# Performance work log

Hardware: AMD Instinct MI355X
Metric: run time of the kernel (lower is better)

Reference implementation:

```python
import jax, jax.numpy as jnp
import numpy as np

MARGIN = 1.0  # cur_margin for LBA_inverted_loss=True
COS_SCALE = 128.0


def smoothed_metric_loss(X, margin=MARGIN):
    # X: [B, E]. Lifted structured loss with inverted cosine similarity.
    B = X.shape[0]
    P = B // 2
    D = (X @ X.T) / COS_SCALE            # [B, B]
    E = jnp.exp(margin + D)              # [B, B]
    # For pair p (rows i=2p, j=2p+1): sum E over rows {i,j}, all columns except {i,j}.
    Eb = E.reshape(P, 2, P, 2)           # [P, 2, P, 2]
    row_sums = Eb.sum(axis=(1, 2, 3))    # [P] full sum over both rows of pair p
    idx = jnp.arange(P)
    diag_block = Eb[idx, :, idx, :].sum(axis=(1, 2))  # [P] the excluded 2x2 block
    S = row_sums - diag_block            # [P] masked sums
    Dij = D.reshape(P, 2, P, 2)[idx, 0, idx, 1]       # [P] D[i, j]
    J = jnp.log(S) - Dij
    return 0.5 * jnp.mean(J * J)


def reference(text_embeddings, shape_embeddings):
    B = text_embeddings.shape[0]
    # shape_embeddings repeated twice per model: row k -> shape[k // 2]
    shape_rep = jnp.repeat(shape_embeddings, 2, axis=0)      # [B, E]
    metric_tt = smoothed_metric_loss(text_embeddings)
    # mask rows: even rows keep text, odd rows take repeated shape embedding
    even = (jnp.arange(B) % 2 == 0)[:, None]
    mixed = jnp.where(even, text_embeddings, shape_rep)      # [B, E]
    metric_st = smoothed_metric_loss(mixed)
    return metric_tt + metric_st


def setup_inputs() -> dict:
    key = jax.random.key(0)
    k1, k2 = jax.random.split(key)
    B, E = 8192, 128
    text_embeddings = jax.random.normal(k1, (B, E), dtype=jnp.float32)
    shape_embeddings = jax.random.normal(k2, (B // 2, E), dtype=jnp.float32)
    return {"text_embeddings": text_embeddings, "shape_embeddings": shape_embeddings}
```

## Files before the change

kernel.cpp:

```cpp
#include <hip/hip_runtime.h>
#include <hip/hip_bf16.h>


#define B_ROWS 8192
#define E_COLS 128
#define P_PAIRS 4096
#define NSTRIP 128
#define NH 8

using f32x4 = __attribute__((ext_vector_type(4))) float;
using i32x8 = __attribute__((ext_vector_type(8))) int;

#define BF_SCALE 0.106164482742544f
#define EULER    2.718281828459045f
#define SCALE1   0x7f

__device__ __forceinline__ unsigned pk4_fp8(float a, float b, float c, float d) {
    unsigned v = 0;
    v = __builtin_amdgcn_cvt_pk_fp8_f32(a * BF_SCALE, b * BF_SCALE, v, false);
    v = __builtin_amdgcn_cvt_pk_fp8_f32(c * BF_SCALE, d * BF_SCALE, v, true);
    return v;
}

__global__ void convert_kernel(const float* __restrict__ text,
                               const float* __restrict__ shape,
                               unsigned* __restrict__ Xt,
                               unsigned* __restrict__ Xm,
                               float* __restrict__ R,
                               float* __restrict__ out) {
    int idx = blockIdx.x * blockDim.x + threadIdx.x;
    if (idx < 4096) {
        float4 z; z.x = z.y = z.z = z.w = 0.f;
        ((float4*)R)[idx] = z;
    }
    if (idx == 0) *out = 0.f;
    int e = idx * 4;
    if (e >= B_ROWS * E_COLS) return;
    float4 t = *(const float4*)(text + e);
    unsigned tp = pk4_fp8(t.x, t.y, t.z, t.w);
    Xt[idx] = tp;
    int row = e >> 7;
    if (row & 1) {
        int col = e & 127;
        float4 s = *(const float4*)(shape + (row >> 1) * E_COLS + col);
        Xm[idx] = pk4_fp8(s.x, s.y, s.z, s.w);
    } else {
        Xm[idx] = tp;
    }
}

__device__ __forceinline__ int lds_off(int row, int k0) {
    return (row << 7) + (k0 ^ ((row & 7) << 4));
}

__device__ __forceinline__ i32x8 load_frag32(const char* base, int row, int k32) {
    union { i32x8 v; int4 h[2]; } u;
    u.h[0] = *(const int4*)(base + lds_off(row, k32));
    u.h[1] = *(const int4*)(base + lds_off(row, k32 + 16));
    return u.v;
}

__device__ __forceinline__ i32x8 load_frag32_g(const char* rowbase, int k32) {
    union { i32x8 v; int4 h[2]; } u;
    u.h[0] = *(const int4*)(rowbase + k32);
    u.h[1] = *(const int4*)(rowbase + k32 + 16);
    return u.v;
}

__device__ __forceinline__ void stage8k(const char* gsrc, char* ldst, int tid) {
#pragma unroll
    for (int it = 0; it < 2; ++it) {
        int L   = it * 4096 + tid * 16;
        int row = L >> 7;
        int cb  = L & 127;
        int src = (row << 7) + (cb ^ ((row & 7) << 4));
        __builtin_amdgcn_global_load_lds(
            (const __attribute__((address_space(1))) void*)(gsrc + src),
            (__attribute__((address_space(3))) void*)(ldst + L), 16, 0, 0);
    }
}

__launch_bounds__(256, 6)
__global__ void gemm_rowsum_kernel(const unsigned char* __restrict__ Xt,
                                   const unsigned char* __restrict__ Xm,
                                   float* __restrict__ R) {
    const int bm = blockIdx.x, h = blockIdx.y, l = blockIdx.z;
    const char* gX = (const char*)(l ? Xm : Xt);

    __shared__ __align__(16) char bufs[3][64 * 128];
    const int tid = threadIdx.x;

    const int t0 = (h == 0) ? NH : h;
    const int N  = (h == 0) ? (bm < 64 ? 8 : 7) : 8;

    stage8k(gX + (size_t)((bm + t0) & 127) * 8192, bufs[0], tid);
    stage8k(gX + (size_t)((bm + t0 + NH) & 127) * 8192, bufs[1], tid);

    const int lane = tid & 63;
    const int w  = tid >> 6;
    const int wr = w >> 1, wc = w & 1;
    const int rA0 = wr * 32 + (lane & 15);
    const int rB0 = wc * 32 + (lane & 15);
    const int k32 = (lane >> 4) * 32;

    const char* Ag = gX + (size_t)bm * 8192;
    i32x8 afr[2];
    afr[0] = load_frag32_g(Ag + (size_t)rA0 * 128, k32);
    afr[1] = load_frag32_g(Ag + (size_t)(rA0 + 16) * 128, k32);

    float s_r[2][4] = {{0.f}};

    if (h == 0) {
        i32x8 b0 = load_frag32_g(Ag + (size_t)rB0 * 128, k32);
        i32x8 b1 = load_frag32_g(Ag + (size_t)(rB0 + 16) * 128, k32);
        f32x4 acc[2][2] = {};
        acc[0][0] = __builtin_amdgcn_mfma_scale_f32_16x16x128_f8f6f4(
            afr[0], b0, acc[0][0], 0, 0, 0, SCALE1, 0, SCALE1);
        acc[0][1] = __builtin_amdgcn_mfma_scale_f32_16x16x128_f8f6f4(
            afr[0], b1, acc[0][1], 0, 0, 0, SCALE1, 0, SCALE1);
        acc[1][0] = __builtin_amdgcn_mfma_scale_f32_16x16x128_f8f6f4(
            afr[1], b0, acc[1][0], 0, 0, 0, SCALE1, 0, SCALE1);
        acc[1][1] = __builtin_amdgcn_mfma_scale_f32_16x16x128_f8f6f4(
            afr[1], b1, acc[1][1], 0, 0, 0, SCALE1, 0, SCALE1);
#pragma unroll
        for (int m = 0; m < 2; ++m)
#pragma unroll
            for (int n = 0; n < 2; ++n)
#pragma unroll
                for (int j = 0; j < 4; ++j)
                    s_r[m][j] += __builtin_amdgcn_exp2f(acc[m][n][j]);
    }

    asm volatile("s_waitcnt vmcnt(0)" ::: "memory");
    __builtin_amdgcn_s_barrier();

    for (int idx = 0; idx < N; ++idx) {
        if (idx + 2 < N)
            stage8k(gX + (size_t)((bm + t0 + NH * (idx + 2)) & 127) * 8192,
                    bufs[(idx + 2) % 3], tid);

        const char* lsrc = bufs[idx % 3];
        i32x8 bfr[2];
        bfr[0] = load_frag32(lsrc, rB0, k32);
        bfr[1] = load_frag32(lsrc, rB0 + 16, k32);

        f32x4 acc[2][2] = {};
        __builtin_amdgcn_s_setprio(1);
        acc[0][0] = __builtin_amdgcn_mfma_scale_f32_16x16x128_f8f6f4(
            afr[0], bfr[0], acc[0][0], 0, 0, 0, SCALE1, 0, SCALE1);
        acc[0][1] = __builtin_amdgcn_mfma_scale_f32_16x16x128_f8f6f4(
            afr[0], bfr[1], acc[0][1], 0, 0, 0, SCALE1, 0, SCALE1);
        acc[1][0] = __builtin_amdgcn_mfma_scale_f32_16x16x128_f8f6f4(
            afr[1], bfr[0], acc[1][0], 0, 0, 0, SCALE1, 0, SCALE1);
        acc[1][1] = __builtin_amdgcn_mfma_scale_f32_16x16x128_f8f6f4(
            afr[1], bfr[1], acc[1][1], 0, 0, 0, SCALE1, 0, SCALE1);
        __builtin_amdgcn_s_setprio(0);

        const int bn = (bm + t0 + NH * idx) & 127;
        float s_c[2] = {0.f, 0.f};
#pragma unroll
        for (int m = 0; m < 2; ++m)
#pragma unroll
            for (int n = 0; n < 2; ++n)
#pragma unroll
                for (int j = 0; j < 4; ++j) {
                    float e2 = __builtin_amdgcn_exp2f(acc[m][n][j]);
                    s_r[m][j] += e2;
                    s_c[n] += e2;
                }
#pragma unroll
        for (int n = 0; n < 2; ++n) {
            float v = s_c[n];
            v += __shfl_xor(v, 16, 64);
            v += __shfl_xor(v, 32, 64);
            if (lane < 16) {
                int gcol = bn * 64 + wc * 32 + n * 16 + lane;
                atomicAdd(&R[l * B_ROWS + gcol], EULER * v);
            }
        }

        if (idx + 1 < N) {
            asm volatile("s_waitcnt lgkmcnt(0)" ::: "memory");
            asm volatile("s_waitcnt vmcnt(4)" ::: "memory");
            __builtin_amdgcn_s_barrier();
        }
    }

#pragma unroll
    for (int m = 0; m < 2; ++m)
#pragma unroll
        for (int j = 0; j < 4; ++j) {
            float v = s_r[m][j];
            v += __shfl_xor(v, 1, 64);
            v += __shfl_xor(v, 2, 64);
            v += __shfl_xor(v, 4, 64);
            v += __shfl_xor(v, 8, 64);
            if ((lane & 15) == 0) {
                int grow = bm * 64 + wr * 32 + m * 16 + (lane >> 4) * 4 + j;
                atomicAdd(&R[l * B_ROWS + grow], EULER * v);
            }
        }
}

__global__ void finalize_kernel(const float* __restrict__ text,
                                const float* __restrict__ shape,
                                const float* __restrict__ R,
                                float* __restrict__ out) {
    const int tid = threadIdx.x;
    const int lane = tid & 63;
    const int w = tid >> 6;
    const int waveGlobal = blockIdx.x * 4 + w;
    const float inv128 = 0.0078125f;
    float accum = 0.f;

    for (int task = waveGlobal; task < 2 * P_PAIRS; task += 2048) {
        int l = task >> 12;
        int p = task & (P_PAIRS - 1);
        const float* a = text + (2 * p) * E_COLS;
        const float* b = l ? (shape + p * E_COLS) : (text + (2 * p + 1) * E_COLS);
        float2 av = *(const float2*)(a + lane * 2);
        float2 bv = *(const float2*)(b + lane * 2);
        float dii = av.x * av.x + av.y * av.y;
        float djj = bv.x * bv.x + bv.y * bv.y;
        float dij = av.x * bv.x + av.y * bv.y;
#pragma unroll
        for (int sh = 1; sh < 64; sh <<= 1) {
            dii += __shfl_xor(dii, sh, 64);
            djj += __shfl_xor(djj, sh, 64);
            dij += __shfl_xor(dij, sh, 64);
        }
        if (lane == 0) {
            float Dii = dii * inv128, Djj = djj * inv128, Dij = dij * inv128;
            float S = R[l * B_ROWS + 2 * p] + R[l * B_ROWS + 2 * p + 1]
                    - (__expf(1.f + Dii) + 2.f * __expf(1.f + Dij) + __expf(1.f + Djj));
            float J = __logf(S) - Dij;
            accum += 0.5f * J * J * (1.0f / (float)P_PAIRS);
        }
    }

    __shared__ float red[4];
    if (lane == 0) red[w] = accum;
    __syncthreads();
    if (tid == 0) {
        atomicAdd(out, red[0] + red[1] + red[2] + red[3]);
    }
}

extern "C" void kernel_launch(void* const* d_in, const int* in_sizes, int n_in,
                              void* d_out, int out_size, void* d_ws, size_t ws_size,
                              hipStream_t stream) {
    const float* text  = (const float*)d_in[0];
    const float* shape = (const float*)d_in[1];
    float* out = (float*)d_out;
    char* ws = (char*)d_ws;

    unsigned char* Xt = (unsigned char*)ws;
    unsigned char* Xm = (unsigned char*)(ws + 1u * 1024u * 1024u);
    float* R = (float*)(ws + 2u * 1024u * 1024u);

    convert_kernel<<<(B_ROWS * E_COLS / 4 + 255) / 256, 256, 0, stream>>>(
        text, shape, (unsigned*)Xt, (unsigned*)Xm, R, out);

    dim3 grid(NSTRIP, NH, 2);
    gemm_rowsum_kernel<<<grid, 256, 0, stream>>>(Xt, Xm, R);

    finalize_kernel<<<512, 256, 0, stream>>>(text, shape, R, out);
}
```

Before: 44.54 us.

## Double-tile LDS stages, fully unroll GEMM loop, defer column-sum atomics

The rowsum GEMM now stages two 64-row tiles per buffer slot across a triple buffer, and runs a fully unrolled four-phase loop with one barrier per pair of tiles. The variable trip count is replaced by a multiplier that zeroes the eighth tile for the blocks that skip it. Column-sum atomics are deferred until after all MFMA work. The aim is fewer barriers and waitcnt stalls and more loads in flight, at the cost of twice the LDS, a lower launch-bound occupancy hint and more live registers. The finalize kernel is also launched with half as many blocks, and the convert kernel's bounds check now runs before it zeroes R.

```diff
diff --git a/kernel.cpp b/kernel.cpp
--- a/kernel.cpp
+++ b/kernel.cpp
@@ -20,6 +20,37 @@
     v = __builtin_amdgcn_cvt_pk_fp8_f32(a * BF_SCALE, b * BF_SCALE, v, false);
     v = __builtin_amdgcn_cvt_pk_fp8_f32(c * BF_SCALE, d * BF_SCALE, v, true);
     return v;
+}
+
+__device__ __forceinline__ int lds_off(int row, int k0) {
+    return (row << 7) + (k0 ^ ((row & 7) << 4));
+}
+
+__device__ __forceinline__ i32x8 load_frag32(const char* base, int row, int k32) {
+    union { i32x8 v; int4 h[2]; } u;
+    u.h[0] = *(const int4*)(base + lds_off(row, k32));
+    u.h[1] = *(const int4*)(base + lds_off(row, k32 + 16));
+    return u.v;
+}
+
+__device__ __forceinline__ i32x8 load_frag32_g(const char* rowbase, int k32) {
+    union { i32x8 v; int4 h[2]; } u;
+    u.h[0] = *(const int4*)(rowbase + k32);
+    u.h[1] = *(const int4*)(rowbase + k32 + 16);
+    return u.v;
+}
+
+__device__ __forceinline__ void stage8k(const char* gsrc, char* ldst, int tid) {
+#pragma unroll
+    for (int it = 0; it < 2; ++it) {
+        int L   = it * 4096 + tid * 16;
+        int row = L >> 7;
+        int cb  = L & 127;
+        int src = (row << 7) + (cb ^ ((row & 7) << 4));
+        __builtin_amdgcn_global_load_lds(
+            (const __attribute__((address_space(1))) void*)(gsrc + src),
+            (__attribute__((address_space(3))) void*)(ldst + L), 16, 0, 0);
+    }
 }
 
 __global__ void convert_kernel(const float* __restrict__ text,
@@ -29,13 +60,13 @@
                                float* __restrict__ R,
                                float* __restrict__ out) {
     int idx = blockIdx.x * blockDim.x + threadIdx.x;
+    if (idx >= B_ROWS * E_COLS / 4) return;
     if (idx < 4096) {
         float4 z; z.x = z.y = z.z = z.w = 0.f;
         ((float4*)R)[idx] = z;
     }
     if (idx == 0) *out = 0.f;
     int e = idx * 4;
-    if (e >= B_ROWS * E_COLS) return;
     float4 t = *(const float4*)(text + e);
     unsigned tp = pk4_fp8(t.x, t.y, t.z, t.w);
     Xt[idx] = tp;
@@ -49,52 +80,18 @@
     }
 }
 
-__device__ __forceinline__ int lds_off(int row, int k0) {
-    return (row << 7) + (k0 ^ ((row & 7) << 4));
-}
-
-__device__ __forceinline__ i32x8 load_frag32(const char* base, int row, int k32) {
-    union { i32x8 v; int4 h[2]; } u;
-    u.h[0] = *(const int4*)(base + lds_off(row, k32));
-    u.h[1] = *(const int4*)(base + lds_off(row, k32 + 16));
-    return u.v;
-}
-
-__device__ __forceinline__ i32x8 load_frag32_g(const char* rowbase, int k32) {
-    union { i32x8 v; int4 h[2]; } u;
-    u.h[0] = *(const int4*)(rowbase + k32);
-    u.h[1] = *(const int4*)(rowbase + k32 + 16);
-    return u.v;
-}
-
-__device__ __forceinline__ void stage8k(const char* gsrc, char* ldst, int tid) {
-#pragma unroll
-    for (int it = 0; it < 2; ++it) {
-        int L   = it * 4096 + tid * 16;
-        int row = L >> 7;
-        int cb  = L & 127;
-        int src = (row << 7) + (cb ^ ((row & 7) << 4));
-        __builtin_amdgcn_global_load_lds(
-            (const __attribute__((address_space(1))) void*)(gsrc + src),
-            (__attribute__((address_space(3))) void*)(ldst + L), 16, 0, 0);
-    }
-}
-
-__launch_bounds__(256, 6)
+__launch_bounds__(256, 3)
 __global__ void gemm_rowsum_kernel(const unsigned char* __restrict__ Xt,
                                    const unsigned char* __restrict__ Xm,
                                    float* __restrict__ R) {
     const int bm = blockIdx.x, h = blockIdx.y, l = blockIdx.z;
     const char* gX = (const char*)(l ? Xm : Xt);
 
-    __shared__ __align__(16) char bufs[3][64 * 128];
+    __shared__ __align__(16) char bufs[3][2][64 * 128];
     const int tid = threadIdx.x;
 
     const int t0 = (h == 0) ? NH : h;
-    const int N  = (h == 0) ? (bm < 64 ? 8 : 7) : 8;
-
-    stage8k(gX + (size_t)((bm + t0) & 127) * 8192, bufs[0], tid);
-    stage8k(gX + (size_t)((bm + t0 + NH) & 127) * 8192, bufs[1], tid);
+    const float g7 = (h == 0 && bm >= 64) ? 0.f : 1.f;
 
     const int lane = tid & 63;
     const int w  = tid >> 6;
@@ -108,20 +105,32 @@
     afr[0] = load_frag32_g(Ag + (size_t)rA0 * 128, k32);
     afr[1] = load_frag32_g(Ag + (size_t)(rA0 + 16) * 128, k32);
 
+    i32x8 db0 = {}, db1 = {};
+    if (h == 0) {
+        db0 = load_frag32_g(Ag + (size_t)rB0 * 128, k32);
+        db1 = load_frag32_g(Ag + (size_t)(rB0 + 16) * 128, k32);
+    }
+
+    stage8k(gX + (size_t)((bm + t0)     & 127) * 8192, bufs[0][0], tid);
+    stage8k(gX + (size_t)((bm + t0 + 8) & 127) * 8192, bufs[0][1], tid);
+    stage8k(gX + (size_t)((bm + t0 + 16) & 127) * 8192, bufs[1][0], tid);
+    stage8k(gX + (size_t)((bm + t0 + 24) & 127) * 8192, bufs[1][1], tid);
+
+    asm volatile("s_waitcnt vmcnt(8)" ::: "memory");
+
     float s_r[2][4] = {{0.f}};
+    float sc[8][2];
 
     if (h == 0) {
-        i32x8 b0 = load_frag32_g(Ag + (size_t)rB0 * 128, k32);
-        i32x8 b1 = load_frag32_g(Ag + (size_t)(rB0 + 16) * 128, k32);
         f32x4 acc[2][2] = {};
         acc[0][0] = __builtin_amdgcn_mfma_scale_f32_16x16x128_f8f6f4(
-            afr[0], b0, acc[0][0], 0, 0, 0, SCALE1, 0, SCALE1);
+            afr[0], db0, acc[0][0], 0, 0, 0, SCALE1, 0, SCALE1);
         acc[0][1] = __builtin_amdgcn_mfma_scale_f32_16x16x128_f8f6f4(
-            afr[0], b1, acc[0][1], 0, 0, 0, SCALE1, 0, SCALE1);
+            afr[0], db1, acc[0][1], 0, 0, 0, SCALE1, 0, SCALE1);
         acc[1][0] = __builtin_amdgcn_mfma_scale_f32_16x16x128_f8f6f4(
-            afr[1], b0, acc[1][0], 0, 0, 0, SCALE1, 0, SCALE1);
+            afr[1], db0, acc[1][0], 0, 0, 0, SCALE1, 0, SCALE1);
         acc[1][1] = __builtin_amdgcn_mfma_scale_f32_16x16x128_f8f6f4(
-            afr[1], b1, acc[1][1], 0, 0, 0, SCALE1, 0, SCALE1);
+            afr[1], db1, acc[1][1], 0, 0, 0, SCALE1, 0, SCALE1);
 #pragma unroll
         for (int m = 0; m < 2; ++m)
 #pragma unroll
@@ -131,58 +140,67 @@
                     s_r[m][j] += __builtin_amdgcn_exp2f(acc[m][n][j]);
     }
 
-    asm volatile("s_waitcnt vmcnt(0)" ::: "memory");
-    __builtin_amdgcn_s_barrier();
-
-    for (int idx = 0; idx < N; ++idx) {
-        if (idx + 2 < N)
-            stage8k(gX + (size_t)((bm + t0 + NH * (idx + 2)) & 127) * 8192,
-                    bufs[(idx + 2) % 3], tid);
-
-        const char* lsrc = bufs[idx % 3];
-        i32x8 bfr[2];
-        bfr[0] = load_frag32(lsrc, rB0, k32);
-        bfr[1] = load_frag32(lsrc, rB0 + 16, k32);
-
-        f32x4 acc[2][2] = {};
-        __builtin_amdgcn_s_setprio(1);
-        acc[0][0] = __builtin_amdgcn_mfma_scale_f32_16x16x128_f8f6f4(
-            afr[0], bfr[0], acc[0][0], 0, 0, 0, SCALE1, 0, SCALE1);
-        acc[0][1] = __builtin_amdgcn_mfma_scale_f32_16x16x128_f8f6f4(
-            afr[0], bfr[1], acc[0][1], 0, 0, 0, SCALE1, 0, SCALE1);
-        acc[1][0] = __builtin_amdgcn_mfma_scale_f32_16x16x128_f8f6f4(
-            afr[1], bfr[0], acc[1][0], 0, 0, 0, SCALE1, 0, SCALE1);
-        acc[1][1] = __builtin_amdgcn_mfma_scale_f32_16x16x128_f8f6f4(
-            afr[1], bfr[1], acc[1][1], 0, 0, 0, SCALE1, 0, SCALE1);
-        __builtin_amdgcn_s_setprio(0);
-
-        const int bn = (bm + t0 + NH * idx) & 127;
-        float s_c[2] = {0.f, 0.f};
-#pragma unroll
-        for (int m = 0; m < 2; ++m)
-#pragma unroll
-            for (int n = 0; n < 2; ++n)
+#pragma unroll
+    for (int p = 0; p < 4; ++p) {
+        if (p < 3) { asm volatile("s_waitcnt vmcnt(4)" ::: "memory"); }
+        else       { asm volatile("s_waitcnt vmcnt(0)" ::: "memory"); }
+        __builtin_amdgcn_s_barrier();
+        if (p + 2 < 4) {
+            stage8k(gX + (size_t)((bm + t0 + 8 * (2 * p + 4)) & 127) * 8192,
+                    bufs[(p + 2) % 3][0], tid);
+            stage8k(gX + (size_t)((bm + t0 + 8 * (2 * p + 5)) & 127) * 8192,
+                    bufs[(p + 2) % 3][1], tid);
+        }
+
+#pragma unroll
+        for (int sub = 0; sub < 2; ++sub) {
+            const int k = 2 * p + sub;
+            const char* lsrc = bufs[p % 3][sub];
+            i32x8 bfr0 = load_frag32(lsrc, rB0, k32);
+            i32x8 bfr1 = load_frag32(lsrc, rB0 + 16, k32);
+
+            f32x4 acc[2][2] = {};
+            __builtin_amdgcn_s_setprio(1);
+            acc[0][0] = __builtin_amdgcn_mfma_scale_f32_16x16x128_f8f6f4(
+                afr[0], bfr0, acc[0][0], 0, 0, 0, SCALE1, 0, SCALE1);
+            acc[0][1] = __builtin_amdgcn_mfma_scale_f32_16x16x128_f8f6f4(
+                afr[0], bfr1, acc[0][1], 0, 0, 0, SCALE1, 0, SCALE1);
+            acc[1][0] = __builtin_amdgcn_mfma_scale_f32_16x16x128_f8f6f4(
+                afr[1], bfr0, acc[1][0], 0, 0, 0, SCALE1, 0, SCALE1);
+            acc[1][1] = __builtin_amdgcn_mfma_scale_f32_16x16x128_f8f6f4(
+                afr[1], bfr1, acc[1][1], 0, 0, 0, SCALE1, 0, SCALE1);
+            __builtin_amdgcn_s_setprio(0);
+
+            const float g = (k == 7) ? g7 : 1.f;
+            float c0 = 0.f, c1 = 0.f;
+#pragma unroll
+            for (int m = 0; m < 2; ++m)
 #pragma unroll
                 for (int j = 0; j < 4; ++j) {
-                    float e2 = __builtin_amdgcn_exp2f(acc[m][n][j]);
-                    s_r[m][j] += e2;
-                    s_c[n] += e2;
+                    float e0 = __builtin_amdgcn_exp2f(acc[m][0][j]) * g;
+                    float e1 = __builtin_amdgcn_exp2f(acc[m][1][j]) * g;
+                    s_r[m][j] += e0 + e1;
+                    c0 += e0;
+                    c1 += e1;
                 }
+            sc[k][0] = c0;
+            sc[k][1] = c1;
+        }
+        asm volatile("s_waitcnt lgkmcnt(0)" ::: "memory");
+    }
+
+#pragma unroll
+    for (int k = 0; k < 8; ++k) {
+        const int bn = (bm + t0 + 8 * k) & 127;
 #pragma unroll
         for (int n = 0; n < 2; ++n) {
-            float v = s_c[n];
+            float v = sc[k][n];
             v += __shfl_xor(v, 16, 64);
             v += __shfl_xor(v, 32, 64);
             if (lane < 16) {
                 int gcol = bn * 64 + wc * 32 + n * 16 + lane;
                 atomicAdd(&R[l * B_ROWS + gcol], EULER * v);
             }
-        }
-
-        if (idx + 1 < N) {
-            asm volatile("s_waitcnt lgkmcnt(0)" ::: "memory");
-            asm volatile("s_waitcnt vmcnt(4)" ::: "memory");
-            __builtin_amdgcn_s_barrier();
         }
     }
 
@@ -209,11 +227,10 @@
     const int tid = threadIdx.x;
     const int lane = tid & 63;
     const int w = tid >> 6;
-    const int waveGlobal = blockIdx.x * 4 + w;
     const float inv128 = 0.0078125f;
     float accum = 0.f;
 
-    for (int task = waveGlobal; task < 2 * P_PAIRS; task += 2048) {
+    for (int task = blockIdx.x * 4 + w; task < 2 * P_PAIRS; task += 1024) {
         int l = task >> 12;
         int p = task & (P_PAIRS - 1);
         const float* a = text + (2 * p) * E_COLS;
@@ -241,9 +258,7 @@
     __shared__ float red[4];
     if (lane == 0) red[w] = accum;
     __syncthreads();
-    if (tid == 0) {
-        atomicAdd(out, red[0] + red[1] + red[2] + red[3]);
-    }
+    if (tid == 0) atomicAdd(out, red[0] + red[1] + red[2] + red[3]);
 }
 
 extern "C" void kernel_launch(void* const* d_in, const int* in_sizes, int n_in,
@@ -264,5 +279,5 @@
     dim3 grid(NSTRIP, NH, 2);
     gemm_rowsum_kernel<<<grid, 256, 0, stream>>>(Xt, Xm, R);
 
-    finalize_kernel<<<512, 256, 0, stream>>>(text, shape, R, out);
-}
+    finalize_kernel<<<256, 256, 0, stream>>>(text, shape, R, out);
+}
```

Measured after the change: 48.28 us. 1.08x slower.

## Repartition tile schedule into six column groups with unrolled pipelined loop

Applied to the files above, without the earlier changes.

The GEMM grid drops from 8 to 6 column groups per strip, so each block handles 10-11 tiles instead of 7-8, with the diagonal tile moved to group 3 and tile 64 given to group 4. The main loop is fully unrolled, with per-iteration vmcnt waits placed before the barrier so loads overlap better and the end-of-iteration barrier goes away. Column-sum atomics are merged into one predicated issue per iteration, and the finalize grid is halved. The aim is to cut block launch and per-block setup overhead and barrier stalls, at the cost of fewer blocks (less parallelism and a possible tail imbalance).

```diff
diff --git a/kernel.cpp b/kernel.cpp
--- a/kernel.cpp
+++ b/kernel.cpp
@@ -6,7 +6,7 @@
 #define E_COLS 128
 #define P_PAIRS 4096
 #define NSTRIP 128
-#define NH 8
+#define NHS 6
 
 using f32x4 = __attribute__((ext_vector_type(4))) float;
 using i32x8 = __attribute__((ext_vector_type(8))) int;
@@ -20,6 +20,37 @@
     v = __builtin_amdgcn_cvt_pk_fp8_f32(a * BF_SCALE, b * BF_SCALE, v, false);
     v = __builtin_amdgcn_cvt_pk_fp8_f32(c * BF_SCALE, d * BF_SCALE, v, true);
     return v;
+}
+
+__device__ __forceinline__ int lds_off(int row, int k0) {
+    return (row << 7) + (k0 ^ ((row & 7) << 4));
+}
+
+__device__ __forceinline__ i32x8 load_frag32(const char* base, int row, int k32) {
+    union { i32x8 v; int4 h[2]; } u;
+    u.h[0] = *(const int4*)(base + lds_off(row, k32));
+    u.h[1] = *(const int4*)(base + lds_off(row, k32 + 16));
+    return u.v;
+}
+
+__device__ __forceinline__ i32x8 load_frag32_g(const char* rowbase, int k32) {
+    union { i32x8 v; int4 h[2]; } u;
+    u.h[0] = *(const int4*)(rowbase + k32);
+    u.h[1] = *(const int4*)(rowbase + k32 + 16);
+    return u.v;
+}
+
+__device__ __forceinline__ void stage8k(const char* gsrc, char* ldst, int tid) {
+#pragma unroll
+    for (int it = 0; it < 2; ++it) {
+        int L   = it * 4096 + tid * 16;
+        int row = L >> 7;
+        int cb  = L & 127;
+        int src = (row << 7) + (cb ^ ((row & 7) << 4));
+        __builtin_amdgcn_global_load_lds(
+            (const __attribute__((address_space(1))) void*)(gsrc + src),
+            (__attribute__((address_space(3))) void*)(ldst + L), 16, 0, 0);
+    }
 }
 
 __global__ void convert_kernel(const float* __restrict__ text,
@@ -29,13 +60,13 @@
                                float* __restrict__ R,
                                float* __restrict__ out) {
     int idx = blockIdx.x * blockDim.x + threadIdx.x;
+    if (idx >= B_ROWS * E_COLS / 4) return;
     if (idx < 4096) {
         float4 z; z.x = z.y = z.z = z.w = 0.f;
         ((float4*)R)[idx] = z;
     }
     if (idx == 0) *out = 0.f;
     int e = idx * 4;
-    if (e >= B_ROWS * E_COLS) return;
     float4 t = *(const float4*)(text + e);
     unsigned tp = pk4_fp8(t.x, t.y, t.z, t.w);
     Xt[idx] = tp;
@@ -49,37 +80,6 @@
     }
 }
 
-__device__ __forceinline__ int lds_off(int row, int k0) {
-    return (row << 7) + (k0 ^ ((row & 7) << 4));
-}
-
-__device__ __forceinline__ i32x8 load_frag32(const char* base, int row, int k32) {
-    union { i32x8 v; int4 h[2]; } u;
-    u.h[0] = *(const int4*)(base + lds_off(row, k32));
-    u.h[1] = *(const int4*)(base + lds_off(row, k32 + 16));
-    return u.v;
-}
-
-__device__ __forceinline__ i32x8 load_frag32_g(const char* rowbase, int k32) {
-    union { i32x8 v; int4 h[2]; } u;
-    u.h[0] = *(const int4*)(rowbase + k32);
-    u.h[1] = *(const int4*)(rowbase + k32 + 16);
-    return u.v;
-}
-
-__device__ __forceinline__ void stage8k(const char* gsrc, char* ldst, int tid) {
-#pragma unroll
-    for (int it = 0; it < 2; ++it) {
-        int L   = it * 4096 + tid * 16;
-        int row = L >> 7;
-        int cb  = L & 127;
-        int src = (row << 7) + (cb ^ ((row & 7) << 4));
-        __builtin_amdgcn_global_load_lds(
-            (const __attribute__((address_space(1))) void*)(gsrc + src),
-            (__attribute__((address_space(3))) void*)(ldst + L), 16, 0, 0);
-    }
-}
-
 __launch_bounds__(256, 6)
 __global__ void gemm_rowsum_kernel(const unsigned char* __restrict__ Xt,
                                    const unsigned char* __restrict__ Xm,
@@ -90,11 +90,11 @@
     __shared__ __align__(16) char bufs[3][64 * 128];
     const int tid = threadIdx.x;
 
-    const int t0 = (h == 0) ? NH : h;
-    const int N  = (h == 0) ? (bm < 64 ? 8 : 7) : 8;
-
-    stage8k(gX + (size_t)((bm + t0) & 127) * 8192, bufs[0], tid);
-    stage8k(gX + (size_t)((bm + t0 + NH) & 127) * 8192, bufs[1], tid);
+    const int t0 = h + 1;
+    int N = (h < 3) ? 11 : 10;
+    if (h == 4 && bm < 64) N = 11;
+
+    auto tf = [&](int i) -> int { return (h == 4 && i == 10) ? 64 : (t0 + 6 * i); };
 
     const int lane = tid & 63;
     const int w  = tid >> 6;
@@ -108,20 +108,29 @@
     afr[0] = load_frag32_g(Ag + (size_t)rA0 * 128, k32);
     afr[1] = load_frag32_g(Ag + (size_t)(rA0 + 16) * 128, k32);
 
+    i32x8 db0 = {}, db1 = {};
+    if (h == 3) {
+        db0 = load_frag32_g(Ag + (size_t)rB0 * 128, k32);
+        db1 = load_frag32_g(Ag + (size_t)(rB0 + 16) * 128, k32);
+    }
+
+    stage8k(gX + (size_t)((bm + tf(0)) & 127) * 8192, bufs[0], tid);
+    stage8k(gX + (size_t)((bm + tf(1)) & 127) * 8192, bufs[1], tid);
+
+    asm volatile("s_waitcnt vmcnt(4)" ::: "memory");
+
     float s_r[2][4] = {{0.f}};
 
-    if (h == 0) {
-        i32x8 b0 = load_frag32_g(Ag + (size_t)rB0 * 128, k32);
-        i32x8 b1 = load_frag32_g(Ag + (size_t)(rB0 + 16) * 128, k32);
+    if (h == 3) {
         f32x4 acc[2][2] = {};
         acc[0][0] = __builtin_amdgcn_mfma_scale_f32_16x16x128_f8f6f4(
-            afr[0], b0, acc[0][0], 0, 0, 0, SCALE1, 0, SCALE1);
+            afr[0], db0, acc[0][0], 0, 0, 0, SCALE1, 0, SCALE1);
         acc[0][1] = __builtin_amdgcn_mfma_scale_f32_16x16x128_f8f6f4(
-            afr[0], b1, acc[0][1], 0, 0, 0, SCALE1, 0, SCALE1);
+            afr[0], db1, acc[0][1], 0, 0, 0, SCALE1, 0, SCALE1);
         acc[1][0] = __builtin_amdgcn_mfma_scale_f32_16x16x128_f8f6f4(
-            afr[1], b0, acc[1][0], 0, 0, 0, SCALE1, 0, SCALE1);
+            afr[1], db0, acc[1][0], 0, 0, 0, SCALE1, 0, SCALE1);
         acc[1][1] = __builtin_amdgcn_mfma_scale_f32_16x16x128_f8f6f4(
-            afr[1], b1, acc[1][1], 0, 0, 0, SCALE1, 0, SCALE1);
+            afr[1], db1, acc[1][1], 0, 0, 0, SCALE1, 0, SCALE1);
 #pragma unroll
         for (int m = 0; m < 2; ++m)
 #pragma unroll
@@ -131,12 +140,18 @@
                     s_r[m][j] += __builtin_amdgcn_exp2f(acc[m][n][j]);
     }
 
-    asm volatile("s_waitcnt vmcnt(0)" ::: "memory");
-    __builtin_amdgcn_s_barrier();
-
-    for (int idx = 0; idx < N; ++idx) {
+#pragma unroll
+    for (int idx = 0; idx < 11; ++idx) {
+        if (idx >= N) break;
+
+        const int vm = ((idx < 2) ? idx : 2) + ((idx + 1 < N) ? 2 : 0);
+        if (vm == 4)      { asm volatile("s_waitcnt vmcnt(4)" ::: "memory"); }
+        else if (vm == 3) { asm volatile("s_waitcnt vmcnt(3)" ::: "memory"); }
+        else              { asm volatile("s_waitcnt vmcnt(2)" ::: "memory"); }
+        __builtin_amdgcn_s_barrier();
+
         if (idx + 2 < N)
-            stage8k(gX + (size_t)((bm + t0 + NH * (idx + 2)) & 127) * 8192,
+            stage8k(gX + (size_t)((bm + tf(idx + 2)) & 127) * 8192,
                     bufs[(idx + 2) % 3], tid);
 
         const char* lsrc = bufs[idx % 3];
@@ -156,7 +171,7 @@
             afr[1], bfr[1], acc[1][1], 0, 0, 0, SCALE1, 0, SCALE1);
         __builtin_amdgcn_s_setprio(0);
 
-        const int bn = (bm + t0 + NH * idx) & 127;
+        const int bn = (bm + tf(idx)) & 127;
         float s_c[2] = {0.f, 0.f};
 #pragma unroll
         for (int m = 0; m < 2; ++m)
@@ -168,22 +183,18 @@
                     s_r[m][j] += e2;
                     s_c[n] += e2;
                 }
-#pragma unroll
-        for (int n = 0; n < 2; ++n) {
-            float v = s_c[n];
-            v += __shfl_xor(v, 16, 64);
-            v += __shfl_xor(v, 32, 64);
-            if (lane < 16) {
-                int gcol = bn * 64 + wc * 32 + n * 16 + lane;
-                atomicAdd(&R[l * B_ROWS + gcol], EULER * v);
-            }
-        }
-
-        if (idx + 1 < N) {
-            asm volatile("s_waitcnt lgkmcnt(0)" ::: "memory");
-            asm volatile("s_waitcnt vmcnt(4)" ::: "memory");
-            __builtin_amdgcn_s_barrier();
-        }
+        float v0 = s_c[0] + __shfl_xor(s_c[0], 16, 64);
+        v0 += __shfl_xor(v0, 32, 64);
+        float v1 = s_c[1] + __shfl_xor(s_c[1], 16, 64);
+        v1 += __shfl_xor(v1, 32, 64);
+        if (lane < 32) {
+            int nn   = lane >> 4;
+            float vv = nn ? v1 : v0;
+            int gcol = bn * 64 + wc * 32 + nn * 16 + (lane & 15);
+            atomicAdd(&R[l * B_ROWS + gcol], EULER * vv);
+        }
+
+        asm volatile("s_waitcnt lgkmcnt(0)" ::: "memory");
     }
 
 #pragma unroll
@@ -209,11 +220,10 @@
     const int tid = threadIdx.x;
     const int lane = tid & 63;
     const int w = tid >> 6;
-    const int waveGlobal = blockIdx.x * 4 + w;
     const float inv128 = 0.0078125f;
     float accum = 0.f;
 
-    for (int task = waveGlobal; task < 2 * P_PAIRS; task += 2048) {
+    for (int task = blockIdx.x * 4 + w; task < 2 * P_PAIRS; task += 1024) {
         int l = task >> 12;
         int p = task & (P_PAIRS - 1);
         const float* a = text + (2 * p) * E_COLS;
@@ -241,9 +251,7 @@
     __shared__ float red[4];
     if (lane == 0) red[w] = accum;
     __syncthreads();
-    if (tid == 0) {
-        atomicAdd(out, red[0] + red[1] + red[2] + red[3]);
-    }
+    if (tid == 0) atomicAdd(out, red[0] + red[1] + red[2] + red[3]);
 }
 
 extern "C" void kernel_launch(void* const* d_in, const int* in_sizes, int n_in,
@@ -261,8 +269,8 @@
     convert_kernel<<<(B_ROWS * E_COLS / 4 + 255) / 256, 256, 0, stream>>>(
         text, shape, (unsigned*)Xt, (unsigned*)Xm, R, out);
 
-    dim3 grid(NSTRIP, NH, 2);
+    dim3 grid(NSTRIP, NHS, 2);
     gemm_rowsum_kernel<<<grid, 256, 0, stream>>>(Xt, Xm, R);
 
-    finalize_kernel<<<512, 256, 0, stream>>>(text, shape, R, out);
-}
+    finalize_kernel<<<256, 256, 0, stream>>>(text, shape, R, out);
+}
```

New measurement: 43.18 us. 3.0% less time.
